# Kernel tuning notes

Measured on AMD Instinct MI355X. Metric: run time of the kernel, lower is better.

## Reference

```python
import jax, jax.numpy as jnp
import numpy as np

DECAY = 0.999
EPS = 1e-05
COMMIT = 0.25


def _layer_norm(x, g, b, eps=1e-5):
    mu = x.mean(-1, keepdims=True)
    var = ((x - mu) ** 2).mean(-1, keepdims=True)
    return (x - mu) * jax.lax.rsqrt(var + eps) * g + b


def setup_inputs() -> dict:
    key = jax.random.key(0)
    ks = jax.random.split(key, 8)
    B, T, D, M, H = 8, 4096, 512, 1024, 512
    init_bound = 1.0 / 512
    embedding = jax.random.uniform(ks[0], (M, D), jnp.float32, -init_bound, init_bound)
    return {
        "dense_x": jax.random.normal(ks[1], (B, T, D), jnp.float32),
        "dense_padding_mask": jax.random.randint(ks[2], (B, T), 0, 2).astype(bool),
        "labels": jax.random.randint(ks[3], (B, T), 0, M),
        "embedding": embedding,
        "ema_count": jnp.zeros((M,), jnp.float32),
        "ema_weight": embedding,
        "ln1_g": jnp.ones((D,), jnp.float32),
        "ln1_b": jnp.zeros((D,), jnp.float32),
        "W1": jax.random.normal(ks[4], (D, H), jnp.float32) * (1.0 / np.sqrt(D)),
        "ln2_g": jnp.ones((H,), jnp.float32),
        "ln2_b": jnp.zeros((H,), jnp.float32),
        "W2": jax.random.normal(ks[5], (H, M), jnp.float32) * (1.0 / np.sqrt(H)),
    }


def reference(dense_x, dense_padding_mask, labels, embedding, ema_count, ema_weight,
              ln1_g, ln1_b, W1, ln2_g, ln2_b, W2):
    B, T, D = dense_x.shape
    M = embedding.shape[0]
    N = B * T

    # ---- VQ codebook (EMA) ----
    x_flat = jax.lax.stop_gradient(dense_x).reshape(N, D)
    distances = (jnp.sum(embedding ** 2, axis=1)[None, :]
                 + jnp.sum(x_flat ** 2, axis=1, keepdims=True)
                 - 2.0 * (x_flat @ embedding.T))
    indices = jnp.argmin(distances, axis=-1)  # [N]
    quantized = embedding[indices].reshape(B, T, D)

    # EMA codebook update (training path); encodings.sum(0) and encodings.T @ x
    # expressed as scatter-adds instead of materializing [N, M] one-hot.
    counts = jnp.zeros((M,), dense_x.dtype).at[indices].add(1.0)
    new_count = DECAY * ema_count + (1.0 - DECAY) * counts
    n = jnp.sum(new_count)
    new_count = (new_count + EPS) / (n + M * EPS) * n
    dw = jnp.zeros((M, D), dense_x.dtype).at[indices].add(x_flat)
    new_weight = DECAY * ema_weight + (1.0 - DECAY) * dw
    new_embedding = new_weight / new_count[:, None]

    e_latent_loss = (dense_x - jax.lax.stop_gradient(quantized)) ** 2  # [B,T,D]
    vq_loss = COMMIT * e_latent_loss
    quantized_st = dense_x + jax.lax.stop_gradient(quantized - dense_x)

    avg_probs = counts / N
    perplexity = jnp.exp(-jnp.sum(avg_probs * jnp.log(avg_probs + 1e-10)))

    # ---- decoder: LN -> ReLU -> Linear -> LN -> ReLU -> Linear ----
    h = jax.nn.relu(_layer_norm(dense_x, ln1_g, ln1_b)) @ W1      # [B,T,H]
    logits = jax.nn.relu(_layer_norm(h, ln2_g, ln2_b)) @ W2       # [B,T,M]

    # ---- cross-entropy with ignore_index=-1 (padding) ----
    lab = jnp.where(dense_padding_mask, -1, labels)
    valid = lab >= 0
    safe = jnp.where(valid, lab, 0)
    logp = jax.nn.log_softmax(logits, axis=-1)
    ce = -jnp.take_along_axis(logp, safe[..., None], axis=-1)[..., 0]
    recon_loss = jnp.where(valid, ce, 0.0)

    loss = recon_loss + vq_loss.sum(-1)  # [B,T]
    return quantized_st, loss, perplexity, new_embedding, new_count, new_weight
```

## Files before the change

kernel.cpp:

```cpp
#include <hip/hip_runtime.h>


#define N_TOK 32768

typedef __attribute__((ext_vector_type(8))) short short8;
typedef _Float16 half8 __attribute__((ext_vector_type(8)));
typedef __attribute__((ext_vector_type(4))) float f32x4;

__device__ __forceinline__ f32x4 mfma16(short8 a, short8 b, f32x4 c) {
    return __builtin_amdgcn_mfma_f32_16x16x32_bf16(a, b, c, 0, 0, 0);
}
__device__ __forceinline__ f32x4 mfma16h(half8 a, half8 b, f32x4 c) {
    return __builtin_amdgcn_mfma_f32_16x16x32_f16(a, b, c, 0, 0, 0);
}

__device__ __forceinline__ void gl_lds16(const void* g, void* l) {
    __builtin_amdgcn_global_load_lds(
        (const __attribute__((address_space(1))) void*)g,
        (__attribute__((address_space(3))) void*)l, 16, 0, 0);
}

__device__ __forceinline__ unsigned short f2bf(float x) {
    unsigned u = __float_as_uint(x);
    u += 0x7fffu + ((u >> 16) & 1u);
    return (unsigned short)(u >> 16);
}
__device__ __forceinline__ float bf2f(unsigned short h) {
    return __uint_as_float(((unsigned)h) << 16);
}
__device__ __forceinline__ unsigned short f2h(float x) {
    union { _Float16 h; unsigned short u; } c;
    c.h = (_Float16)x;
    return c.u;
}
__device__ __forceinline__ float h2f(unsigned short u) {
    union { _Float16 h; unsigned short u; } c;
    c.u = u;
    return (float)c.h;
}

__device__ __forceinline__ float waveSum(float v) {
#pragma unroll
    for (int off = 32; off > 0; off >>= 1) v += __shfl_down(v, off, 64);
    return v;
}
__device__ __forceinline__ float xorSum(float v) {
#pragma unroll
    for (int off = 1; off < 64; off <<= 1) v += __shfl_xor(v, off);
    return v;
}

__device__ __forceinline__ void stage_tile128(const unsigned short* __restrict__ src,
                                              int r0, int k0, short* lds,
                                              int w, int lane) {
#pragma unroll
    for (int iss = 0; iss < 2; ++iss) {
        int L = (w << 11) + (iss << 10) + (lane << 4);
        int kb = L >> 11, m = (L >> 4) & 127;
        gl_lds16(src + (((size_t)(r0 + m)) << 9) + k0 + (kb << 3), (char*)lds + L);
    }
}

__global__ __launch_bounds__(256) void prep_x_kernel(
        const float* __restrict__ X, const float* __restrict__ g,
        const float* __restrict__ b, unsigned short* __restrict__ Xf,
        unsigned short* __restrict__ A1, unsigned long long* __restrict__ minpack) {
    int tid = threadIdx.x;
    if (tid < 4) minpack[(blockIdx.x << 2) + tid] = ~0ULL;
    int lane = tid & 63;
    int n = (blockIdx.x << 2) + (tid >> 6);
    const float* row = X + ((size_t)n << 9);
    float v[8]; float s = 0.f, ss = 0.f;
#pragma unroll
    for (int i = 0; i < 8; ++i) { v[i] = row[lane + (i << 6)]; s += v[i]; ss += v[i] * v[i]; }
    s = xorSum(s); ss = xorSum(ss);
    float mu = s * (1.f / 512.f);
    float rs = rsqrtf(ss * (1.f / 512.f) - mu * mu + 1e-5f);
#pragma unroll
    for (int i = 0; i < 8; ++i) {
        int c = lane + (i << 6);
        size_t o = ((size_t)n << 9) + c;
        float x = v[i];
        Xf[o] = f2h(x);
        float a = fmaxf((x - mu) * rs * g[c] + b[c], 0.f);
        A1[o] = f2bf(a);
    }
}

__global__ __launch_bounds__(256) void prep_h_kernel(
        const unsigned short* __restrict__ Hb, const float* __restrict__ g,
        const float* __restrict__ b, unsigned short* __restrict__ A2) {
    int lane = threadIdx.x & 63;
    int n = (blockIdx.x << 2) + (threadIdx.x >> 6);
    const unsigned short* row = Hb + ((size_t)n << 9);
    float v[8]; float s = 0.f, ss = 0.f;
#pragma unroll
    for (int i = 0; i < 8; ++i) { v[i] = bf2f(row[lane + (i << 6)]); s += v[i]; ss += v[i] * v[i]; }
    s = xorSum(s); ss = xorSum(ss);
    float mu = s * (1.f / 512.f);
    float rs = rsqrtf(ss * (1.f / 512.f) - mu * mu + 1e-5f);
#pragma unroll
    for (int i = 0; i < 8; ++i) {
        int c = lane + (i << 6);
        float a = fmaxf((v[i] - mu) * rs * g[c] + b[c], 0.f);
        A2[((size_t)n << 9) + c] = f2bf(a);
    }
}

__global__ __launch_bounds__(256) void prep_e_kernel(
        const float* __restrict__ E, unsigned short* __restrict__ Ehf,
        unsigned short* __restrict__ Elf, float* __restrict__ e_sq,
        int* __restrict__ izero) {
    if (blockIdx.x < 8) izero[(blockIdx.x << 8) + threadIdx.x] = 0;
    int lane = threadIdx.x & 63;
    int m = (blockIdx.x << 2) + (threadIdx.x >> 6);
    const float* row = E + ((size_t)m << 9);
    float ss = 0.f;
#pragma unroll
    for (int i = 0; i < 8; ++i) {
        int c = lane + (i << 6);
        float x = row[c];
        ss += x * x;
        float xs = x * 512.f;
        unsigned short h = f2h(xs);
        size_t o = ((size_t)m << 9) + c;
        Ehf[o] = h;
        Elf[o] = f2h(xs - h2f(h));
    }
    ss = xorSum(ss);
    if (lane == 0) e_sq[m] = ss * 512.f;
}

__global__ __launch_bounds__(256) void prep_wt_kernel(
        const float* __restrict__ W1, const float* __restrict__ W2,
        unsigned short* __restrict__ W1T, unsigned short* __restrict__ W2T) {
    __shared__ float t[32][33];
    int bx = blockIdx.x;
    const float* W = (bx < 16) ? W1 : W2;
    unsigned short* WT = (bx < 16) ? W1T : W2T;
    int Nw = (bx < 16) ? 512 : 1024;
    int n0 = ((bx < 16) ? bx : (bx - 16)) << 5, k0 = blockIdx.y << 5;
    int tx = threadIdx.x & 31, ty = threadIdx.x >> 5;
#pragma unroll
    for (int l = 0; l < 4; ++l)
        t[ty + (l << 3)][tx] = W[(size_t)(k0 + ty + (l << 3)) * Nw + n0 + tx];
    __syncthreads();
#pragma unroll
    for (int l = 0; l < 4; ++l)
        WT[(((size_t)(n0 + ty + (l << 3))) << 9) + k0 + tx] = f2bf(t[tx][ty + (l << 3)]);
}

__device__ __forceinline__ unsigned long long packDist(float d, int m) {
    unsigned u = __float_as_uint(d);
    u = (u & 0x80000000u) ? ~u : (u | 0x80000000u);
    return ((unsigned long long)u << 32) | (unsigned)m;
}

__global__ __launch_bounds__(256) void dist_mfma_kernel(
        const unsigned short* __restrict__ Xf,
        const unsigned short* __restrict__ Ehf, const unsigned short* __restrict__ Elf,
        const float* __restrict__ e_sq, unsigned long long* __restrict__ minpack) {
    __shared__ __align__(16) short Axs[4096];
    int tid = threadIdx.x, lane = tid & 63, w = tid >> 6;
    int quad = lane >> 4, lanelo = lane & 15;
    int wm = w >> 1, wn = w & 1;
    int row0 = blockIdx.x << 7, m0 = blockIdx.y << 7;
    f32x4 acc[4][4];
#pragma unroll
    for (int i = 0; i < 4; ++i)
#pragma unroll
        for (int j = 0; j < 4; ++j) acc[i][j] = 0.f;

    size_t boff[4];
#pragma unroll
    for (int j = 0; j < 4; ++j) {
        int code = m0 + (wn << 6) + (j << 4) + lanelo;
        boff[j] = ((size_t)code << 9) + (quad << 3);
    }

    for (int k0 = 0; k0 < 512; k0 += 32) {
        stage_tile128(Xf, row0, k0, Axs, w, lane);
        half8 bh[4], bl[4];
#pragma unroll
        for (int j = 0; j < 4; ++j) {
            bh[j] = __builtin_bit_cast(half8, *(const short8*)(Ehf + boff[j] + k0));
            bl[j] = __builtin_bit_cast(half8, *(const short8*)(Elf + boff[j] + k0));
        }
        __syncthreads();
        half8 av[4];
#pragma unroll
        for (int i = 0; i < 4; ++i) {
            int m = (wm << 6) + (i << 4) + lanelo;
            av[i] = __builtin_bit_cast(half8, *(const short8*)&Axs[(quad << 10) + (m << 3)]);
        }
#pragma unroll
        for (int i = 0; i < 4; ++i)
#pragma unroll
            for (int j = 0; j < 4; ++j) {
                acc[i][j] = mfma16h(av[i], bh[j], acc[i][j]);
                acc[i][j] = mfma16h(av[i], bl[j], acc[i][j]);
            }
        __syncthreads();
    }

    float esq[4];
#pragma unroll
    for (int j = 0; j < 4; ++j) esq[j] = e_sq[m0 + (wn << 6) + (j << 4) + lanelo];
#pragma unroll
    for (int i = 0; i < 4; ++i)
#pragma unroll
        for (int r = 0; r < 4; ++r) {
            unsigned long long best = ~0ULL;
#pragma unroll
            for (int j = 0; j < 4; ++j) {
                int code = m0 + (wn << 6) + (j << 4) + lanelo;
                float d = esq[j] - 2.f * acc[i][j][r];
                unsigned long long p = packDist(d, code);
                if (p < best) best = p;
            }
#pragma unroll
            for (int off = 1; off < 16; off <<= 1) {
                unsigned long long q = __shfl_xor(best, off);
                if (q < best) best = q;
            }
            if (lanelo == 0) {
                int t = row0 + (wm << 6) + (i << 4) + (quad << 2) + r;
                atomicMin(&minpack[t], best);
            }
        }
}

__global__ __launch_bounds__(256) void gather_kernel(
        const float* __restrict__ X, const float* __restrict__ E,
        const unsigned long long* __restrict__ minpack,
        float* __restrict__ out_q, int* __restrict__ icounts,
        float* __restrict__ vqsum) {
    int lane = threadIdx.x & 63;
    int n = (blockIdx.x << 2) + (threadIdx.x >> 6);
    int idx = (int)(minpack[n] & 0xFFFFFFFFULL);
    if (lane == 0) atomicAdd(&icounts[idx], 1);
    const float* xr = X + ((size_t)n << 9);
    const float* er = E + ((size_t)idx << 9);
    float s = 0.f;
#pragma unroll
    for (int i = 0; i < 8; ++i) {
        int c = lane + (i << 6);
        float xv = xr[c], q = er[c];
        out_q[((size_t)n << 9) + c] = q;
        float dlt = xv - q;
        s += dlt * dlt;
    }
    s = waveSum(s);
    if (lane == 0) vqsum[n] = 0.25f * s;
}

__global__ __launch_bounds__(1024) void codebook_kernel(
        const float* __restrict__ ema_count, const int* __restrict__ icounts,
        float* __restrict__ out_perp, float* __restrict__ out_newcount,
        int* __restrict__ offsets) {
    __shared__ int sc[1024];
    __shared__ float red[16];
    int tid = threadIdx.x;
    int lane = tid & 63, wid = tid >> 6;
    int ic = icounts[tid];
    sc[tid] = ic;
    for (int off = 1; off < 1024; off <<= 1) {
        __syncthreads();
        int v = (tid >= off) ? sc[tid - off] : 0;
        __syncthreads();
        sc[tid] += v;
    }
    offsets[tid] = sc[tid] - ic;
    __syncthreads();

    float cnt = (float)ic;
    float raw = 0.999f * ema_count[tid] + 0.001f * cnt;
    float v = waveSum(raw);
    if (lane == 0) red[wid] = v;
    __syncthreads();
    float nsum = 0.f;
#pragma unroll
    for (int i = 0; i < 16; ++i) nsum += red[i];
    __syncthreads();
    float p = cnt * (1.f / 32768.f);
    float e = p * logf(p + 1e-10f);
    e = waveSum(e);
    if (lane == 0) red[wid] = e;
    __syncthreads();
    float ent = 0.f;
#pragma unroll
    for (int i = 0; i < 16; ++i) ent += red[i];
    float nc = (raw + 1e-5f) / (nsum + 1024.f * 1e-5f) * nsum;
    out_newcount[tid] = nc;
    if (tid == 0) out_perp[0] = expf(-ent);
}

__global__ __launch_bounds__(256) void scatter_kernel(
        const unsigned long long* __restrict__ minpack,
        const int* __restrict__ offsets, int* __restrict__ cursor,
        int* __restrict__ bucket) {
    int n = (blockIdx.x << 8) + threadIdx.x;
    int idx = (int)(minpack[n] & 0xFFFFFFFFULL);
    int pos = atomicAdd(&cursor[idx], 1);
    bucket[offsets[idx] + pos] = n;
}

__global__ __launch_bounds__(256) void dw_kernel(
        const float* __restrict__ X, const int* __restrict__ bucket,
        const int* __restrict__ icounts, const int* __restrict__ offsets,
        float* __restrict__ dw) {
    __shared__ float comb[4][512];
    int tid = threadIdx.x, lane = tid & 63, w = tid >> 6;
    int m = blockIdx.x;
    int cnt = icounts[m], base = offsets[m];
    float acc[8] = {};
    for (int i = w; i < cnt; i += 4) {
        int t = bucket[base + i];
        const float* xr = X + ((size_t)t << 9);
#pragma unroll
        for (int j = 0; j < 8; ++j) acc[j] += xr[lane + (j << 6)];
    }
#pragma unroll
    for (int j = 0; j < 8; ++j) comb[w][lane + (j << 6)] = acc[j];
    __syncthreads();
    for (int c = tid; c < 512; c += 256)
        dw[((size_t)m << 9) + c] = comb[0][c] + comb[1][c] + comb[2][c] + comb[3][c];
}

__global__ __launch_bounds__(256) void gemm1_mfma_kernel(
        const unsigned short* __restrict__ A1, const unsigned short* __restrict__ W1T,
        unsigned short* __restrict__ Hb) {
    __shared__ __align__(16) short As[4096];
    int tid = threadIdx.x, lane = tid & 63, w = tid >> 6;
    int quad = lane >> 4, lanelo = lane & 15;
    int wm = w >> 1, wn = w & 1;
    int row0 = blockIdx.x << 7, n0 = blockIdx.y << 7;
    f32x4 acc[4][4];
#pragma unroll
    for (int i = 0; i < 4; ++i)
#pragma unroll
        for (int j = 0; j < 4; ++j) acc[i][j] = 0.f;

    size_t boff[4];
#pragma unroll
    for (int j = 0; j < 4; ++j)
        boff[j] = ((size_t)(n0 + (wn << 6) + (j << 4) + lanelo) << 9) + (quad << 3);

    for (int k0 = 0; k0 < 512; k0 += 32) {
        stage_tile128(A1, row0, k0, As, w, lane);
        short8 bf[4];
#pragma unroll
        for (int j = 0; j < 4; ++j) bf[j] = *(const short8*)(W1T + boff[j] + k0);
        __syncthreads();
        short8 af[4];
#pragma unroll
        for (int i = 0; i < 4; ++i) {
            int m = (wm << 6) + (i << 4) + lanelo;
            af[i] = *(const short8*)&As[(quad << 10) + (m << 3)];
        }
#pragma unroll
        for (int i = 0; i < 4; ++i)
#pragma unroll
            for (int j = 0; j < 4; ++j) acc[i][j] = mfma16(af[i], bf[j], acc[i][j]);
        __syncthreads();
    }
#pragma unroll
    for (int i = 0; i < 4; ++i)
#pragma unroll
        for (int j = 0; j < 4; ++j)
#pragma unroll
            for (int r = 0; r < 4; ++r) {
                int row = row0 + (wm << 6) + (i << 4) + (quad << 2) + r;
                int col = n0 + (wn << 6) + (j << 4) + lanelo;
                Hb[((size_t)row << 9) + col] = f2bf(acc[i][j][r]);
            }
}

__global__ __launch_bounds__(256) void gemm2_chunk_kernel(
        const unsigned short* __restrict__ A2, const unsigned short* __restrict__ W2T,
        const int* __restrict__ mask, const int* __restrict__ labels,
        float* __restrict__ ws_cmax, float* __restrict__ ws_csum,
        float* __restrict__ ws_lab) {
    __shared__ __align__(16) short As[4096];
    __shared__ float lmax[2][2][64], lsum[2][2][64], llab[128];
    __shared__ int slab[128];
    int tid = threadIdx.x, lane = tid & 63, w = tid >> 6;
    int quad = lane >> 4, lanelo = lane & 15;
    int wm = w >> 1, wn = w & 1;
    int row0 = blockIdx.x << 7, c0 = blockIdx.y << 7;
    if (tid < 128) {
        int mk = mask[row0 + tid];
        slab[tid] = mk ? 0 : labels[row0 + tid];
    }
    f32x4 acc[4][4];
#pragma unroll
    for (int i = 0; i < 4; ++i)
#pragma unroll
        for (int j = 0; j < 4; ++j) acc[i][j] = 0.f;

    size_t boff[4];
#pragma unroll
    for (int j = 0; j < 4; ++j)
        boff[j] = ((size_t)(c0 + (wn << 6) + (j << 4) + lanelo) << 9) + (quad << 3);

    for (int k0 = 0; k0 < 512; k0 += 32) {
        stage_tile128(A2, row0, k0, As, w, lane);
        short8 bf[4];
#pragma unroll
        for (int j = 0; j < 4; ++j) bf[j] = *(const short8*)(W2T + boff[j] + k0);
        __syncthreads();
        short8 af[4];
#pragma unroll
        for (int i = 0; i < 4; ++i) {
            int m = (wm << 6) + (i << 4) + lanelo;
            af[i] = *(const short8*)&As[(quad << 10) + (m << 3)];
        }
#pragma unroll
        for (int i = 0; i < 4; ++i)
#pragma unroll
            for (int j = 0; j < 4; ++j) acc[i][j] = mfma16(af[i], bf[j], acc[i][j]);
        __syncthreads();
    }

#pragma unroll
    for (int i = 0; i < 4; ++i)
#pragma unroll
        for (int j = 0; j < 4; ++j)
#pragma unroll
            for (int r = 0; r < 4; ++r) {
                int code = c0 + (wn << 6) + (j << 4) + lanelo;
                int tt = (wm << 6) + (i << 4) + (quad << 2) + r;
                if (code == slab[tt]) llab[tt] = acc[i][j][r];
            }
#pragma unroll
    for (int i = 0; i < 4; ++i)
#pragma unroll
        for (int r = 0; r < 4; ++r) {
            float mx = fmaxf(fmaxf(acc[i][0][r], acc[i][1][r]),
                             fmaxf(acc[i][2][r], acc[i][3][r]));
#pragma unroll
            for (int off = 1; off < 16; off <<= 1) mx = fmaxf(mx, __shfl_xor(mx, off));
            if (lanelo == 0) lmax[wm][wn][(i << 4) + (quad << 2) + r] = mx;
        }
    __syncthreads();
#pragma unroll
    for (int i = 0; i < 4; ++i)
#pragma unroll
        for (int r = 0; r < 4; ++r) {
            int tl = (i << 4) + (quad << 2) + r;
            float cm = fmaxf(lmax[wm][0][tl], lmax[wm][1][tl]);
            float s = expf(acc[i][0][r] - cm) + expf(acc[i][1][r] - cm) +
                      expf(acc[i][2][r] - cm) + expf(acc[i][3][r] - cm);
#pragma unroll
            for (int off = 1; off < 16; off <<= 1) s += __shfl_xor(s, off);
            if (lanelo == 0) lsum[wm][wn][tl] = s;
        }
    __syncthreads();
    if (tid < 128) {
        int wmi = tid >> 6, tl = tid & 63;
        int token = row0 + tid;
        float cm = fmaxf(lmax[wmi][0][tl], lmax[wmi][1][tl]);
        float cs = lsum[wmi][0][tl] + lsum[wmi][1][tl];
        size_t o = ((size_t)blockIdx.y << 15) + token;
        ws_cmax[o] = cm;
        ws_csum[o] = cs;
        if ((slab[tid] >> 7) == (int)blockIdx.y) ws_lab[token] = llab[tid];
    }
}

__global__ __launch_bounds__(256) void epilogue_kernel(
        const float* __restrict__ ema_weight, const float* __restrict__ dw,
        const float* __restrict__ newcount, float* __restrict__ out_neww,
        float* __restrict__ out_newemb,
        const float* __restrict__ ws_cmax, const float* __restrict__ ws_csum,
        const float* __restrict__ ws_lab, const int* __restrict__ mask,
        const float* __restrict__ vqsum, float* __restrict__ loss_out) {
    int bx = blockIdx.x;
    if (bx < 2048) {
        int i = (bx << 8) + threadIdx.x;
        float nw = 0.999f * ema_weight[i] + 0.001f * dw[i];
        out_neww[i] = nw;
        out_newemb[i] = nw / newcount[i >> 9];
    } else {
        int n = ((bx - 2048) << 8) + threadIdx.x;
        float m[8], s[8];
#pragma unroll
        for (int c = 0; c < 8; ++c) {
            m[c] = ws_cmax[(c << 15) + n];
            s[c] = ws_csum[(c << 15) + n];
        }
        float gm = m[0];
#pragma unroll
        for (int c = 1; c < 8; ++c) gm = fmaxf(gm, m[c]);
        float se = 0.f;
#pragma unroll
        for (int c = 0; c < 8; ++c) se += s[c] * expf(m[c] - gm);
        float ce = -(ws_lab[n] - gm - logf(se));
        loss_out[n] = (mask[n] ? 0.f : ce) + vqsum[n];
    }
}

extern "C" void kernel_launch(void* const* d_in, const int* in_sizes, int n_in,
                              void* d_out, int out_size, void* d_ws, size_t ws_size,
                              hipStream_t stream) {
    const float* X          = (const float*)d_in[0];
    const int*   mask       = (const int*)d_in[1];
    const int*   labels     = (const int*)d_in[2];
    const float* E          = (const float*)d_in[3];
    const float* ema_count  = (const float*)d_in[4];
    const float* ema_weight = (const float*)d_in[5];
    const float* g1 = (const float*)d_in[6];
    const float* b1 = (const float*)d_in[7];
    const float* W1 = (const float*)d_in[8];
    const float* g2 = (const float*)d_in[9];
    const float* b2 = (const float*)d_in[10];
    const float* W2 = (const float*)d_in[11];

    float* out = (float*)d_out;
    float* out_q        = out;
    float* out_loss     = out + 16777216;
    float* out_perp     = out + 16809984;
    float* out_newemb   = out + 16809985;
    float* out_newcount = out + 17334273;
    float* out_neww     = out + 17335297;

    float* w = (float*)d_ws;
    float* vqsum = w;  w += 32768;
    float* e_sq = w;   w += 1024;
    float* dwbuf = w;  w += 524288;
    unsigned long long* minpack = (unsigned long long*)w; w += 65536;
    float* ws_cmax = w; w += 262144;
    float* ws_csum = w; w += 262144;
    float* ws_lab  = w; w += 32768;
    int* icounts = (int*)w; w += 1024;
    int* cursor  = (int*)w; w += 1024;
    int* offsets = (int*)w; w += 1024;
    int* bucket  = (int*)w; w += 32768;
    unsigned short* Ehf = (unsigned short*)w; w += 262144;
    unsigned short* Elf = (unsigned short*)w; w += 262144;
    unsigned short* W1T = (unsigned short*)w; w += 131072;
    unsigned short* W2T = (unsigned short*)w; w += 262144;
    unsigned short* Xf  = (unsigned short*)w; w += 8388608;
    unsigned short* A1  = (unsigned short*)w; w += 8388608;
    unsigned short* Hb  = (unsigned short*)w; w += 8388608;
    unsigned short* A2  = Xf;

    prep_e_kernel<<<256, 256, 0, stream>>>(E, Ehf, Elf, e_sq, icounts);
    prep_wt_kernel<<<dim3(48, 16), 256, 0, stream>>>(W1, W2, W1T, W2T);
    prep_x_kernel<<<8192, 256, 0, stream>>>(X, g1, b1, Xf, A1, minpack);
    dist_mfma_kernel<<<dim3(256, 8), 256, 0, stream>>>(Xf, Ehf, Elf, e_sq, minpack);
    gather_kernel<<<8192, 256, 0, stream>>>(X, E, minpack, out_q, icounts, vqsum);
    codebook_kernel<<<1, 1024, 0, stream>>>(ema_count, icounts, out_perp,
                                            out_newcount, offsets);
    scatter_kernel<<<128, 256, 0, stream>>>(minpack, offsets, cursor, bucket);
    dw_kernel<<<1024, 256, 0, stream>>>(X, bucket, icounts, offsets, dwbuf);
    gemm1_mfma_kernel<<<dim3(256, 4), 256, 0, stream>>>(A1, W1T, Hb);
    prep_h_kernel<<<8192, 256, 0, stream>>>(Hb, g2, b2, A2);
    gemm2_chunk_kernel<<<dim3(256, 8), 256, 0, stream>>>(A2, W2T, mask, labels,
                                                         ws_cmax, ws_csum, ws_lab);
    epilogue_kernel<<<2176, 256, 0, stream>>>(ema_weight, dwbuf, out_newcount,
                                              out_neww, out_newemb,
                                              ws_cmax, ws_csum, ws_lab,
                                              mask, vqsum, out_loss);
}
```

Measured before the change: 560.4 us.

## Double-buffer A and B tiles in LDS with async prefetch in MFMA GEMMs

The three MFMA GEMM kernels (distance, gemm1, gemm2) now stage both the A and B operand tiles into LDS through global_load_lds, using a two-stage ping-pong buffer. The next k-slice is prefetched while the current one is consumed, and manual vmcnt waits plus raw barriers replace __syncthreads. B fragments are now read from LDS instead of directly from global memory per lane. The aim is to hide global-load latency behind MFMA work, at the cost of more LDS per block (up to 48KB in the distance kernel), which may lower occupancy. It also relies on the hand-set waitcnt counts matching the number of loads issued by stage_tile128.

```diff
diff --git a/kernel.cpp b/kernel.cpp
--- a/kernel.cpp
+++ b/kernel.cpp
@@ -2,6 +2,8 @@
 
 
 #define N_TOK 32768
+#define WAITV(n) __builtin_amdgcn_s_waitcnt(0x0F70 | (n))
+#define BAR() __builtin_amdgcn_s_barrier()
 
 typedef __attribute__((ext_vector_type(8))) short short8;
 typedef _Float16 half8 __attribute__((ext_vector_type(8)));
@@ -160,7 +162,7 @@
         const unsigned short* __restrict__ Xf,
         const unsigned short* __restrict__ Ehf, const unsigned short* __restrict__ Elf,
         const float* __restrict__ e_sq, unsigned long long* __restrict__ minpack) {
-    __shared__ __align__(16) short Axs[4096];
+    __shared__ __align__(16) short L[2][3][4096];
     int tid = threadIdx.x, lane = tid & 63, w = tid >> 6;
     int quad = lane >> 4, lanelo = lane & 15;
     int wm = w >> 1, wn = w & 1;
@@ -171,27 +173,33 @@
 #pragma unroll
         for (int j = 0; j < 4; ++j) acc[i][j] = 0.f;
 
-    size_t boff[4];
-#pragma unroll
-    for (int j = 0; j < 4; ++j) {
-        int code = m0 + (wn << 6) + (j << 4) + lanelo;
-        boff[j] = ((size_t)code << 9) + (quad << 3);
-    }
-
-    for (int k0 = 0; k0 < 512; k0 += 32) {
-        stage_tile128(Xf, row0, k0, Axs, w, lane);
-        half8 bh[4], bl[4];
-#pragma unroll
-        for (int j = 0; j < 4; ++j) {
-            bh[j] = __builtin_bit_cast(half8, *(const short8*)(Ehf + boff[j] + k0));
-            bl[j] = __builtin_bit_cast(half8, *(const short8*)(Elf + boff[j] + k0));
-        }
-        __syncthreads();
-        half8 av[4];
+    stage_tile128(Xf, row0, 0, L[0][0], w, lane);
+    stage_tile128(Ehf, m0, 0, L[0][1], w, lane);
+    stage_tile128(Elf, m0, 0, L[0][2], w, lane);
+
+    for (int it = 0; it < 16; ++it) {
+        if (it < 15) {
+            int kn = (it + 1) << 5, nb = (it + 1) & 1;
+            stage_tile128(Xf, row0, kn, L[nb][0], w, lane);
+            stage_tile128(Ehf, m0, kn, L[nb][1], w, lane);
+            stage_tile128(Elf, m0, kn, L[nb][2], w, lane);
+            WAITV(6);
+        } else {
+            WAITV(0);
+        }
+        BAR();
+        int cb = it & 1;
+        half8 av[4], bh[4], bl[4];
 #pragma unroll
         for (int i = 0; i < 4; ++i) {
             int m = (wm << 6) + (i << 4) + lanelo;
-            av[i] = __builtin_bit_cast(half8, *(const short8*)&Axs[(quad << 10) + (m << 3)]);
+            av[i] = __builtin_bit_cast(half8, *(const short8*)&L[cb][0][(quad << 10) + (m << 3)]);
+        }
+#pragma unroll
+        for (int j = 0; j < 4; ++j) {
+            int n = (wn << 6) + (j << 4) + lanelo;
+            bh[j] = __builtin_bit_cast(half8, *(const short8*)&L[cb][1][(quad << 10) + (n << 3)]);
+            bl[j] = __builtin_bit_cast(half8, *(const short8*)&L[cb][2][(quad << 10) + (n << 3)]);
         }
 #pragma unroll
         for (int i = 0; i < 4; ++i)
@@ -200,7 +208,7 @@
                 acc[i][j] = mfma16h(av[i], bh[j], acc[i][j]);
                 acc[i][j] = mfma16h(av[i], bl[j], acc[i][j]);
             }
-        __syncthreads();
+        BAR();
     }
 
     float esq[4];
@@ -330,7 +338,7 @@
 __global__ __launch_bounds__(256) void gemm1_mfma_kernel(
         const unsigned short* __restrict__ A1, const unsigned short* __restrict__ W1T,
         unsigned short* __restrict__ Hb) {
-    __shared__ __align__(16) short As[4096];
+    __shared__ __align__(16) short L[2][2][4096];
     int tid = threadIdx.x, lane = tid & 63, w = tid >> 6;
     int quad = lane >> 4, lanelo = lane & 15;
     int wm = w >> 1, wn = w & 1;
@@ -341,28 +349,36 @@
 #pragma unroll
         for (int j = 0; j < 4; ++j) acc[i][j] = 0.f;
 
-    size_t boff[4];
-#pragma unroll
-    for (int j = 0; j < 4; ++j)
-        boff[j] = ((size_t)(n0 + (wn << 6) + (j << 4) + lanelo) << 9) + (quad << 3);
-
-    for (int k0 = 0; k0 < 512; k0 += 32) {
-        stage_tile128(A1, row0, k0, As, w, lane);
-        short8 bf[4];
-#pragma unroll
-        for (int j = 0; j < 4; ++j) bf[j] = *(const short8*)(W1T + boff[j] + k0);
-        __syncthreads();
-        short8 af[4];
+    stage_tile128(A1, row0, 0, L[0][0], w, lane);
+    stage_tile128(W1T, n0, 0, L[0][1], w, lane);
+
+    for (int it = 0; it < 16; ++it) {
+        if (it < 15) {
+            int kn = (it + 1) << 5, nb = (it + 1) & 1;
+            stage_tile128(A1, row0, kn, L[nb][0], w, lane);
+            stage_tile128(W1T, n0, kn, L[nb][1], w, lane);
+            WAITV(4);
+        } else {
+            WAITV(0);
+        }
+        BAR();
+        int cb = it & 1;
+        short8 af[4], bf[4];
 #pragma unroll
         for (int i = 0; i < 4; ++i) {
             int m = (wm << 6) + (i << 4) + lanelo;
-            af[i] = *(const short8*)&As[(quad << 10) + (m << 3)];
+            af[i] = *(const short8*)&L[cb][0][(quad << 10) + (m << 3)];
+        }
+#pragma unroll
+        for (int j = 0; j < 4; ++j) {
+            int n = (wn << 6) + (j << 4) + lanelo;
+            bf[j] = *(const short8*)&L[cb][1][(quad << 10) + (n << 3)];
         }
 #pragma unroll
         for (int i = 0; i < 4; ++i)
 #pragma unroll
             for (int j = 0; j < 4; ++j) acc[i][j] = mfma16(af[i], bf[j], acc[i][j]);
-        __syncthreads();
+        BAR();
     }
 #pragma unroll
     for (int i = 0; i < 4; ++i)
@@ -381,7 +397,7 @@
         const int* __restrict__ mask, const int* __restrict__ labels,
         float* __restrict__ ws_cmax, float* __restrict__ ws_csum,
         float* __restrict__ ws_lab) {
-    __shared__ __align__(16) short As[4096];
+    __shared__ __align__(16) short L[2][2][4096];
     __shared__ float lmax[2][2][64], lsum[2][2][64], llab[128];
     __shared__ int slab[128];
     int tid = threadIdx.x, lane = tid & 63, w = tid >> 6;
@@ -392,34 +408,43 @@
         int mk = mask[row0 + tid];
         slab[tid] = mk ? 0 : labels[row0 + tid];
     }
+    __syncthreads();
     f32x4 acc[4][4];
 #pragma unroll
     for (int i = 0; i < 4; ++i)
 #pragma unroll
         for (int j = 0; j < 4; ++j) acc[i][j] = 0.f;
 
-    size_t boff[4];
-#pragma unroll
-    for (int j = 0; j < 4; ++j)
-        boff[j] = ((size_t)(c0 + (wn << 6) + (j << 4) + lanelo) << 9) + (quad << 3);
-
-    for (int k0 = 0; k0 < 512; k0 += 32) {
-        stage_tile128(A2, row0, k0, As, w, lane);
-        short8 bf[4];
-#pragma unroll
-        for (int j = 0; j < 4; ++j) bf[j] = *(const short8*)(W2T + boff[j] + k0);
-        __syncthreads();
-        short8 af[4];
+    stage_tile128(A2, row0, 0, L[0][0], w, lane);
+    stage_tile128(W2T, c0, 0, L[0][1], w, lane);
+
+    for (int it = 0; it < 16; ++it) {
+        if (it < 15) {
+            int kn = (it + 1) << 5, nb = (it + 1) & 1;
+            stage_tile128(A2, row0, kn, L[nb][0], w, lane);
+            stage_tile128(W2T, c0, kn, L[nb][1], w, lane);
+            WAITV(4);
+        } else {
+            WAITV(0);
+        }
+        BAR();
+        int cb = it & 1;
+        short8 af[4], bf[4];
 #pragma unroll
         for (int i = 0; i < 4; ++i) {
             int m = (wm << 6) + (i << 4) + lanelo;
-            af[i] = *(const short8*)&As[(quad << 10) + (m << 3)];
+            af[i] = *(const short8*)&L[cb][0][(quad << 10) + (m << 3)];
+        }
+#pragma unroll
+        for (int j = 0; j < 4; ++j) {
+            int n = (wn << 6) + (j << 4) + lanelo;
+            bf[j] = *(const short8*)&L[cb][1][(quad << 10) + (n << 3)];
         }
 #pragma unroll
         for (int i = 0; i < 4; ++i)
 #pragma unroll
             for (int j = 0; j < 4; ++j) acc[i][j] = mfma16(af[i], bf[j], acc[i][j]);
-        __syncthreads();
+        BAR();
     }
 
 #pragma unroll
```

Measured after the change: 477.8 us. 14.7% less time.
